# Optimization experiments

Hardware: AMD Instinct MI355X
Metric: run time of the kernel (lower is better)

Reference implementation:

```python
import jax, jax.numpy as jnp
import numpy as np

N_HEADS = 8
HEAD_SIZE = 64
CONTEXT = 256
D_MODEL = 512
MASK_NEG = 1e9


def setup_inputs() -> dict:
    key = jax.random.key(0)
    k1, k2, k3, k4 = jax.random.split(key, 4)
    B, T, D = 2, 4096, D_MODEL
    # Glorot-uniform-ish scales
    def glorot(k, shape):
        fan_in, fan_out = shape[-2], shape[-1]
        lim = jnp.sqrt(6.0 / (fan_in + fan_out))
        return jax.random.uniform(k, shape, jnp.float32, -lim, lim)
    inputs = jax.random.normal(k1, (B, T, D), dtype=jnp.float32)
    WQ = glorot(k2, (N_HEADS, D, HEAD_SIZE))
    WV = glorot(k3, (N_HEADS, D, HEAD_SIZE))
    WU = glorot(k4, (N_HEADS * HEAD_SIZE, D))
    return {"inputs": inputs, "WQ": WQ, "WV": WV, "WU": WU}


def reference(inputs, WQ, WV, WU):
    B, T, D = inputs.shape
    H, _, S = WQ.shape
    # Q, V: [B, H, T, hs]
    Q = jnp.einsum('btd,hds->bhts', inputs, WQ)
    V = jnp.einsum('btd,hds->bhts', inputs, WV)
    # Scores use Q @ V^T (no separate K in this module): [B, H, T, T]
    scores = jnp.einsum('bhts,bhus->bhtu', Q, V) / jnp.sqrt(jnp.float32(S))
    idx = jnp.arange(T)
    band = jnp.abs(idx[:, None] - idx[None, :]) <= CONTEXT  # [T, T] bool
    scores = scores - MASK_NEG * (~band).astype(scores.dtype)
    W = jax.nn.softmax(scores, axis=-1)
    C = jnp.einsum('bhtu,bhus->bhts', W, V)  # [B, H, T, hs]
    # concat heads along feature dim: [B, T, H*hs]
    C = C.transpose(0, 2, 1, 3).reshape(B, T, H * S)
    return C @ WU  # [B, T, D]
```

## Files before the change

### kernel.cpp

```cpp
#include <hip/hip_runtime.h>

#define TSEQ 4096
#define DM 512
#define NH 8
#define HS 64
#define CTX 256

typedef __attribute__((ext_vector_type(8))) short bf16x8;
typedef __attribute__((ext_vector_type(4))) float f32x4;
typedef unsigned short u16;
typedef unsigned long long ull;

__device__ __forceinline__ u16 f2bf(float x) {
    unsigned u = __float_as_uint(x);
    unsigned r = (u + 0x7fffu + ((u >> 16) & 1u)) >> 16;
    return (u16)r;
}
__device__ __forceinline__ float bf2f(u16 b) {
    return __uint_as_float(((unsigned)b) << 16);
}
__device__ __forceinline__ unsigned bf16dup(float p) {
    unsigned w;
    asm("v_cvt_pk_bf16_f32 %0, %1, %1" : "=v"(w) : "v"(p));
    return w;
}
template<int CTRL>
__device__ __forceinline__ float dpp_ror(float x) {
    int xi = __float_as_int(x);
    return __int_as_float(__builtin_amdgcn_update_dpp(xi, xi, CTRL, 0xf, 0xf, false));
}
__device__ __forceinline__ float row16_max(float v) {
    v = fmaxf(v, dpp_ror<0x121>(v));
    v = fmaxf(v, dpp_ror<0x122>(v));
    v = fmaxf(v, dpp_ror<0x124>(v));
    v = fmaxf(v, dpp_ror<0x128>(v));
    return v;
}

#define MFMA(a, b, c) __builtin_amdgcn_mfma_f32_16x16x32_bf16((a), (b), (c), 0, 0, 0)

__global__ __launch_bounds__(256) void presplit_xw(
    const float* __restrict__ X,
    const float* __restrict__ WQ, const float* __restrict__ WV,
    const float* __restrict__ WU,
    u16* __restrict__ Xh,
    u16* __restrict__ WQt_h, u16* __restrict__ WVt_h, u16* __restrict__ WUt_h)
{
    int b = blockIdx.x;
    if (b < 2048) {
        size_t idx = ((size_t)b * 256 + threadIdx.x) * 8;
        float4 p0 = *(const float4*)(X + idx);
        float4 p1 = *(const float4*)(X + idx + 4);
        float v[8] = {p0.x, p0.y, p0.z, p0.w, p1.x, p1.y, p1.z, p1.w};
        bf16x8 h;
        #pragma unroll
        for (int i = 0; i < 8; ++i) h[i] = (short)f2bf(v[i]);
        *(bf16x8*)(Xh + idx) = h;
    } else {
        int gidx = (b - 2048) * 256 + threadIdx.x;
        int a = gidx >> 18;
        int r = gidx & 262143;
        float val;
        u16* dh;
        int dst;
        if (a < 2) {
            int h = r >> 15, s = (r >> 9) & 63, d = r & 511;
            const float* W = (a == 0) ? WQ : WV;
            val = W[h * 32768 + d * 64 + s];
            dst = h * 32768 + s * 512 + d;
            dh = (a == 0) ? WQt_h : WVt_h;
        } else {
            int n = r >> 9, k = r & 511;
            val = WU[k * 512 + n];
            dst = n * 512 + k;
            dh = WUt_h;
        }
        dh[dst] = f2bf(val);
    }
}

__global__ __launch_bounds__(256) void gemm_qv(
    const u16* __restrict__ Ah_g,
    const u16* __restrict__ B0h, const u16* __restrict__ B1h,
    u16* __restrict__ O0h,
    u16* __restrict__ O1h,
    u16* __restrict__ O1t)
{
    __shared__ u16 Ah[128][64];
    __shared__ u16 Bh[64][64];

    const int tid = threadIdx.x;
    const int w = tid >> 6, lane = tid & 63;
    const int lg = lane >> 4, ln = lane & 15;
    const int r0 = blockIdx.x * 128;
    const int y = blockIdx.y;

    const u16* Bsh = (y < 8) ? B0h + (size_t)y * 32768
                             : B1h + (size_t)(y - 8) * 32768;

    const int r_a = tid >> 3;
    const int kc  = tid & 7;
    const int wcol = (kc * 8) ^ ((r_a & 7) << 3);
    const size_t gA = (size_t)(r0 + r_a) * DM + kc * 8;
    const size_t gB = (size_t)r_a * 512 + kc * 8;

    bf16x8 a0h, a1h, a2h, a3h, b0h, b1h;

    #define GLOAD(k0)                                                   \
        a0h = *(const bf16x8*)(Ah_g + gA + (k0));                       \
        a1h = *(const bf16x8*)(Ah_g + gA + 32 * DM + (k0));             \
        a2h = *(const bf16x8*)(Ah_g + gA + 64 * DM + (k0));             \
        a3h = *(const bf16x8*)(Ah_g + gA + 96 * DM + (k0));             \
        b0h = *(const bf16x8*)(Bsh + gB + (k0));                        \
        b1h = *(const bf16x8*)(Bsh + gB + 32 * 512 + (k0));

    f32x4 acc[2][4];
    #pragma unroll
    for (int i = 0; i < 2; ++i)
        #pragma unroll
        for (int j = 0; j < 4; ++j)
            acc[i][j] = (f32x4){0.f, 0.f, 0.f, 0.f};

    GLOAD(0);

    for (int kt = 0; kt < 8; ++kt) {
        __syncthreads();
        *(bf16x8*)&Ah[r_a][wcol]      = a0h;
        *(bf16x8*)&Ah[r_a + 32][wcol] = a1h;
        *(bf16x8*)&Ah[r_a + 64][wcol] = a2h;
        *(bf16x8*)&Ah[r_a + 96][wcol] = a3h;
        *(bf16x8*)&Bh[r_a][wcol]      = b0h;
        *(bf16x8*)&Bh[r_a + 32][wcol] = b1h;
        __syncthreads();
        if (kt < 7) { GLOAD((kt + 1) * 64); }

        #pragma unroll
        for (int kk = 0; kk < 2; ++kk) {
            const int fc = (kk * 32 + lg * 8) ^ ((ln & 7) << 3);
            bf16x8 ah[2], bh2[4];
            #pragma unroll
            for (int ti = 0; ti < 2; ++ti)
                ah[ti] = *(const bf16x8*)&Ah[w * 32 + ti * 16 + ln][fc];
            #pragma unroll
            for (int nj = 0; nj < 4; ++nj)
                bh2[nj] = *(const bf16x8*)&Bh[nj * 16 + ln][fc];
            #pragma unroll
            for (int ti = 0; ti < 2; ++ti)
                #pragma unroll
                for (int nj = 0; nj < 4; ++nj)
                    acc[ti][nj] = MFMA(ah[ti], bh2[nj], acc[ti][nj]);
        }
    }
    #undef GLOAD

    const float qscale = (y < 8) ? 0.18033688f : 1.0f;
    #pragma unroll
    for (int ti = 0; ti < 2; ++ti)
        #pragma unroll
        for (int nj = 0; nj < 4; ++nj) {
            u16 hb[4];
            #pragma unroll
            for (int r = 0; r < 4; ++r) {
                float val = acc[ti][nj][r] * qscale;
                hb[r] = f2bf(val);
                int t = r0 + w * 32 + ti * 16 + lg * 4 + r;
                int n = nj * 16 + ln;
                int bh = (t >> 12) * NH + (y & 7);
                size_t off = ((size_t)bh * TSEQ + (t & (TSEQ - 1))) * HS + n;
                if (y < 8) O0h[off] = hb[r];
                else       O1h[off] = hb[r];
            }
            if (y >= 8) {
                int t = r0 + w * 32 + ti * 16 + lg * 4;
                int n = nj * 16 + ln;
                int bh = (t >> 12) * NH + (y & 7);
                size_t off = (size_t)bh * TSEQ * HS + (size_t)n * TSEQ + (t & (TSEQ - 1));
                ull pk = (ull)hb[0] | ((ull)hb[1] << 16)
                       | ((ull)hb[2] << 32) | ((ull)hb[3] << 48);
                *(ull*)(O1t + off) = pk;
            }
        }
}

__global__ __launch_bounds__(256) void gemm_out(
    const u16* __restrict__ Ah_g, const u16* __restrict__ Bt_h,
    float* __restrict__ Of)
{
    __shared__ u16 Ah[64][64];
    __shared__ u16 Bh[64][64];

    const int tid = threadIdx.x;
    const int w = tid >> 6, lane = tid & 63;
    const int lg = lane >> 4, ln = lane & 15;
    const int r0 = blockIdx.x * 64;
    const int y = blockIdx.y;

    const u16* Bsh = Bt_h + (size_t)y * 64 * 512;

    const int r_a = tid >> 3;
    const int kc  = tid & 7;
    const int wcol = (kc * 8) ^ ((r_a & 7) << 3);
    const size_t gA = (size_t)(r0 + r_a) * DM + kc * 8;
    const size_t gB = (size_t)r_a * 512 + kc * 8;

    bf16x8 a0h, a1h, b0h, b1h;

    #define GLOAD(k0)                                                   \
        a0h = *(const bf16x8*)(Ah_g + gA + (k0));                       \
        a1h = *(const bf16x8*)(Ah_g + gA + 32 * DM + (k0));             \
        b0h = *(const bf16x8*)(Bsh + gB + (k0));                        \
        b1h = *(const bf16x8*)(Bsh + gB + 32 * 512 + (k0));

    f32x4 acc[4];
    #pragma unroll
    for (int j = 0; j < 4; ++j)
        acc[j] = (f32x4){0.f, 0.f, 0.f, 0.f};

    GLOAD(0);

    for (int kt = 0; kt < 8; ++kt) {
        __syncthreads();
        *(bf16x8*)&Ah[r_a][wcol]      = a0h;
        *(bf16x8*)&Ah[r_a + 32][wcol] = a1h;
        *(bf16x8*)&Bh[r_a][wcol]      = b0h;
        *(bf16x8*)&Bh[r_a + 32][wcol] = b1h;
        __syncthreads();
        if (kt < 7) { GLOAD((kt + 1) * 64); }

        #pragma unroll
        for (int kk = 0; kk < 2; ++kk) {
            const int fc = (kk * 32 + lg * 8) ^ ((ln & 7) << 3);
            bf16x8 ah = *(const bf16x8*)&Ah[w * 16 + ln][fc];
            bf16x8 bh2[4];
            #pragma unroll
            for (int nj = 0; nj < 4; ++nj)
                bh2[nj] = *(const bf16x8*)&Bh[nj * 16 + ln][fc];
            #pragma unroll
            for (int nj = 0; nj < 4; ++nj)
                acc[nj] = MFMA(ah, bh2[nj], acc[nj]);
        }
    }
    #undef GLOAD

    #pragma unroll
    for (int nj = 0; nj < 4; ++nj)
        #pragma unroll
        for (int r = 0; r < 4; ++r) {
            int t = r0 + w * 16 + lg * 4 + r;
            Of[(size_t)t * DM + y * 64 + nj * 16 + ln] = acc[nj][r];
        }
}

__global__ __launch_bounds__(256) void attn_v11(
    const u16* __restrict__ Qh_g,
    const u16* __restrict__ Vnh_g, const u16* __restrict__ Vth_g,
    u16* __restrict__ Ch)
{
    __shared__ u16 Vn_h[2][64][64];
    __shared__ u16 Vt_h[2][64][64];
    __shared__ unsigned Ps[4][16][32];

    const int tid = threadIdx.x;
    const int w = tid >> 6, lane = tid & 63;
    const int lg = lane >> 4, ln = lane & 15;
    const int raw = blockIdx.x;
    const int swz = (raw & 7) * 128 + (raw >> 3);
    const int ttile = swz & 63;
    const int bh = swz >> 6;
    const int t0 = ttile * 64;
    const size_t base = (size_t)bh * TSEQ * HS;
    const u16* Qph = Qh_g + base;
    const u16* Vph = Vnh_g + base;
    const u16* Vth = Vth_g + base;

    bf16x8 qh[2];
    #pragma unroll
    for (int kk = 0; kk < 2; ++kk) {
        size_t off = (size_t)(t0 + w * 16 + ln) * HS + kk * 32 + lg * 8;
        qh[kk] = *(const bf16x8*)(Qph + off);
    }

    bf16x8 ones_frag;
    #pragma unroll
    for (int e = 0; e < 8; ++e)
        ones_frag[e] = (ln == 0) ? (short)0x3F80 : (short)0;

    f32x4 o[4], o4;
    float m[4];
    #pragma unroll
    for (int j = 0; j < 4; ++j) {
        o[j] = (f32x4){0.f, 0.f, 0.f, 0.f};
        m[j] = -1e30f;
    }
    o4 = (f32x4){0.f, 0.f, 0.f, 0.f};

    int u_lo = t0 - CTX; if (u_lo < 0) u_lo = 0;
    int u_hi = t0 + 64 + CTX; if (u_hi > TSEQ) u_hi = TSEQ;

    const int sr = tid >> 3;
    const int c8 = (tid & 7) * 8;
    const int wcA = c8 ^ ((sr & 7) << 3);

    bf16x8 vn0h, vn1h, vt0h, vt1h;
    #define VL(u0v)                                                             \
        vn0h = *(const bf16x8*)(Vph + (size_t)((u0v) + sr) * HS + c8);          \
        vn1h = *(const bf16x8*)(Vph + (size_t)((u0v) + sr + 32) * HS + c8);     \
        vt0h = *(const bf16x8*)(Vth + (size_t)sr * TSEQ + (u0v) + c8);          \
        vt1h = *(const bf16x8*)(Vth + (size_t)(sr + 32) * TSEQ + (u0v) + c8);
    #define VSTORE(bufi)                                                        \
        *(bf16x8*)&Vn_h[bufi][sr][wcA]      = vn0h;                             \
        *(bf16x8*)&Vn_h[bufi][sr + 32][wcA] = vn1h;                             \
        *(bf16x8*)&Vt_h[bufi][sr][wcA]      = vt0h;                             \
        *(bf16x8*)&Vt_h[bufi][sr + 32][wcA] = vt1h;

    VL(u_lo);
    VSTORE(0);
    __syncthreads();

    int cur = 0;
    for (int u0 = u_lo; u0 < u_hi; u0 += 64) {
        const bool more = (u0 + 64 < u_hi);
        if (more) { VL(u0 + 64); }

        f32x4 s[4];
        #pragma unroll
        for (int j = 0; j < 4; ++j) s[j] = (f32x4){0.f, 0.f, 0.f, 0.f};

        #pragma unroll
        for (int kk = 0; kk < 2; ++kk) {
            const int fc = (kk * 32 + lg * 8) ^ ((ln & 7) << 3);
            bf16x8 vh[4];
            #pragma unroll
            for (int uj = 0; uj < 4; ++uj)
                vh[uj] = *(const bf16x8*)&Vn_h[cur][uj * 16 + ln][fc];
            #pragma unroll
            for (int uj = 0; uj < 4; ++uj)
                s[uj] = MFMA(qh[kk], vh[uj], s[uj]);
        }

        bool needmask = ((t0 + 63 - u0) > CTX) || ((u0 + 63 - t0) > CTX);
        if (needmask) {
            #pragma unroll
            for (int uj = 0; uj < 4; ++uj)
                #pragma unroll
                for (int r = 0; r < 4; ++r) {
                    int t = t0 + w * 16 + lg * 4 + r;
                    int u = u0 + uj * 16 + ln;
                    int d = t - u; if (d < 0) d = -d;
                    if (d > CTX) s[uj][r] = -1e30f;
                }
        }

        float rm[4];
        bool need = false;
        #pragma unroll
        for (int r = 0; r < 4; ++r) {
            float v = fmaxf(fmaxf(s[0][r], s[1][r]), fmaxf(s[2][r], s[3][r]));
            rm[r] = row16_max(v);
            need |= (rm[r] > m[r] + 8.f);
        }
        if (__any(need)) {
            #pragma unroll
            for (int r = 0; r < 4; ++r) {
                float mn = fmaxf(m[r], rm[r]);
                float sc2 = exp2f(m[r] - mn);
                m[r] = mn;
                o4[r] *= sc2;
                #pragma unroll
                for (int sj = 0; sj < 4; ++sj)
                    o[sj][r] *= sc2;
            }
        }
        #pragma unroll
        for (int r = 0; r < 4; ++r)
            #pragma unroll
            for (int uj = 0; uj < 4; ++uj)
                s[uj][r] = exp2f(s[uj][r] - m[r]);

        #pragma unroll
        for (int kk = 0; kk < 2; ++kk) {
            #pragma unroll
            for (int u2 = 0; u2 < 2; ++u2) {
                int uj = kk * 2 + u2;
                #pragma unroll
                for (int r = 0; r < 4; ++r) {
                    int trow = lg * 4 + r;
                    int ucol = (u2 * 16 + ln) ^ ((trow & 7) << 2);
                    Ps[w][trow][ucol] = bf16dup(s[uj][r]);
                }
            }

            bf16x8 ph, vth4[4];
            {
                int sw = (ln & 7) << 2;
                uint4 q0 = *(const uint4*)&Ps[w][ln][(lg * 8) ^ sw];
                uint4 q1 = *(const uint4*)&Ps[w][ln][(lg * 8 + 4) ^ sw];
                union { unsigned u[4]; bf16x8 v; } H;
                H.u[0] = __builtin_amdgcn_perm(q0.y, q0.x, 0x05040100u);
                H.u[1] = __builtin_amdgcn_perm(q0.w, q0.z, 0x05040100u);
                H.u[2] = __builtin_amdgcn_perm(q1.y, q1.x, 0x05040100u);
                H.u[3] = __builtin_amdgcn_perm(q1.w, q1.z, 0x05040100u);
                ph = H.v;
            }
            const int fct = (kk * 32 + lg * 8) ^ ((ln & 7) << 3);
            #pragma unroll
            for (int sj = 0; sj < 4; ++sj)
                vth4[sj] = *(const bf16x8*)&Vt_h[cur][sj * 16 + ln][fct];
            #pragma unroll
            for (int sj = 0; sj < 4; ++sj)
                o[sj] = MFMA(ph, vth4[sj], o[sj]);
            o4 = MFMA(ph, ones_frag, o4);
        }

        if (more) { VSTORE(cur ^ 1); }
        __syncthreads();
        cur ^= 1;
    }
    #undef VL
    #undef VSTORE

    const int b = bh >> 3, h = bh & 7;
    #pragma unroll
    for (int r = 0; r < 4; ++r) {
        float ls = __shfl(o4[r], (lane >> 4) << 4);
        float inv = 1.f / ls;
        int t = t0 + w * 16 + lg * 4 + r;
        #pragma unroll
        for (int sj = 0; sj < 4; ++sj) {
            int ss = sj * 16 + ln;
            float val = o[sj][r] * inv;
            size_t off = ((size_t)(b * TSEQ + t)) * DM + h * HS + ss;
            Ch[off] = f2bf(val);
        }
    }
}

extern "C" void kernel_launch(void* const* d_in, const int* in_sizes, int n_in,
                              void* d_out, int out_size, void* d_ws, size_t ws_size,
                              hipStream_t stream) {
    const float* X  = (const float*)d_in[0];
    const float* WQ = (const float*)d_in[1];
    const float* WV = (const float*)d_in[2];
    const float* WU = (const float*)d_in[3];
    float* out = (float*)d_out;

    const size_t SZ = 8388608;
    char* ws = (char*)d_ws;

    u16* Xh = (u16*)(ws);
    u16* Qh = (u16*)(ws + 2 * SZ);
    u16* Vh = (u16*)(ws + 4 * SZ);
    u16* Vth = (u16*)(ws + 6 * SZ);
    char* wsw = ws + 8 * SZ;
    u16* WQt_h = (u16*)(wsw);
    u16* WVt_h = (u16*)(wsw + 524288);
    u16* WUt_h = (u16*)(wsw + 2 * 524288);

    presplit_xw<<<5120, 256, 0, stream>>>(X, WQ, WV, WU, Xh, WQt_h, WVt_h, WUt_h);
    gemm_qv<<<dim3(64, 16), 256, 0, stream>>>(Xh, WQt_h, WVt_h, Qh, Vh, Vth);
    attn_v11<<<1024, 256, 0, stream>>>(Qh, Vh, Vth, Xh);
    gemm_out<<<dim3(128, 8), 256, 0, stream>>>(Xh, WUt_h, out);
}
```

Baseline: 72.17 us.

## Compute Q and V projections in one block sharing the X tile

The Q/V projection GEMM is reorganized so each block loads a 64-row X tile once and multiplies it against both the WQ and WV head slices, instead of launching separate blocks for Q and V that each reload 128 X rows. The grid becomes 128x8 with smaller row tiles, and each wave computes 16 rows times 64 columns for both Q and V. This is meant to halve X tile traffic and remove the divergent branches in the epilogue. The cost is less A-fragment reuse per wave across row tiles and more LDS traffic for B fragments.

```diff
diff --git a/kernel.cpp b/kernel.cpp
--- a/kernel.cpp
+++ b/kernel.cpp
@@ -79,24 +79,25 @@
     }
 }
 
-__global__ __launch_bounds__(256) void gemm_qv(
+__global__ __launch_bounds__(256) void gemm_qv2(
     const u16* __restrict__ Ah_g,
-    const u16* __restrict__ B0h, const u16* __restrict__ B1h,
-    u16* __restrict__ O0h,
-    u16* __restrict__ O1h,
-    u16* __restrict__ O1t)
+    const u16* __restrict__ BQ, const u16* __restrict__ BV,
+    u16* __restrict__ Qh,
+    u16* __restrict__ Vh,
+    u16* __restrict__ Vt)
 {
-    __shared__ u16 Ah[128][64];
-    __shared__ u16 Bh[64][64];
+    __shared__ u16 Ah[64][64];
+    __shared__ u16 Bq[64][64];
+    __shared__ u16 Bv[64][64];
 
     const int tid = threadIdx.x;
     const int w = tid >> 6, lane = tid & 63;
     const int lg = lane >> 4, ln = lane & 15;
-    const int r0 = blockIdx.x * 128;
+    const int r0 = blockIdx.x * 64;
     const int y = blockIdx.y;
 
-    const u16* Bsh = (y < 8) ? B0h + (size_t)y * 32768
-                             : B1h + (size_t)(y - 8) * 32768;
+    const u16* Bq_g = BQ + (size_t)y * 32768;
+    const u16* Bv_g = BV + (size_t)y * 32768;
 
     const int r_a = tid >> 3;
     const int kc  = tid & 7;
@@ -104,22 +105,22 @@
     const size_t gA = (size_t)(r0 + r_a) * DM + kc * 8;
     const size_t gB = (size_t)r_a * 512 + kc * 8;
 
-    bf16x8 a0h, a1h, a2h, a3h, b0h, b1h;
+    bf16x8 a0h, a1h, q0h, q1h, v0h, v1h;
 
     #define GLOAD(k0)                                                   \
         a0h = *(const bf16x8*)(Ah_g + gA + (k0));                       \
         a1h = *(const bf16x8*)(Ah_g + gA + 32 * DM + (k0));             \
-        a2h = *(const bf16x8*)(Ah_g + gA + 64 * DM + (k0));             \
-        a3h = *(const bf16x8*)(Ah_g + gA + 96 * DM + (k0));             \
-        b0h = *(const bf16x8*)(Bsh + gB + (k0));                        \
-        b1h = *(const bf16x8*)(Bsh + gB + 32 * 512 + (k0));
-
-    f32x4 acc[2][4];
-    #pragma unroll
-    for (int i = 0; i < 2; ++i)
-        #pragma unroll
-        for (int j = 0; j < 4; ++j)
-            acc[i][j] = (f32x4){0.f, 0.f, 0.f, 0.f};
+        q0h = *(const bf16x8*)(Bq_g + gB + (k0));                       \
+        q1h = *(const bf16x8*)(Bq_g + gB + 32 * 512 + (k0));            \
+        v0h = *(const bf16x8*)(Bv_g + gB + (k0));                       \
+        v1h = *(const bf16x8*)(Bv_g + gB + 32 * 512 + (k0));
+
+    f32x4 accq[4], accv[4];
+    #pragma unroll
+    for (int j = 0; j < 4; ++j) {
+        accq[j] = (f32x4){0.f, 0.f, 0.f, 0.f};
+        accv[j] = (f32x4){0.f, 0.f, 0.f, 0.f};
+    }
 
     GLOAD(0);
 
@@ -127,59 +128,57 @@
         __syncthreads();
         *(bf16x8*)&Ah[r_a][wcol]      = a0h;
         *(bf16x8*)&Ah[r_a + 32][wcol] = a1h;
-        *(bf16x8*)&Ah[r_a + 64][wcol] = a2h;
-        *(bf16x8*)&Ah[r_a + 96][wcol] = a3h;
-        *(bf16x8*)&Bh[r_a][wcol]      = b0h;
-        *(bf16x8*)&Bh[r_a + 32][wcol] = b1h;
+        *(bf16x8*)&Bq[r_a][wcol]      = q0h;
+        *(bf16x8*)&Bq[r_a + 32][wcol] = q1h;
+        *(bf16x8*)&Bv[r_a][wcol]      = v0h;
+        *(bf16x8*)&Bv[r_a + 32][wcol] = v1h;
         __syncthreads();
         if (kt < 7) { GLOAD((kt + 1) * 64); }
 
         #pragma unroll
         for (int kk = 0; kk < 2; ++kk) {
             const int fc = (kk * 32 + lg * 8) ^ ((ln & 7) << 3);
-            bf16x8 ah[2], bh2[4];
-            #pragma unroll
-            for (int ti = 0; ti < 2; ++ti)
-                ah[ti] = *(const bf16x8*)&Ah[w * 32 + ti * 16 + ln][fc];
-            #pragma unroll
-            for (int nj = 0; nj < 4; ++nj)
-                bh2[nj] = *(const bf16x8*)&Bh[nj * 16 + ln][fc];
-            #pragma unroll
-            for (int ti = 0; ti < 2; ++ti)
-                #pragma unroll
-                for (int nj = 0; nj < 4; ++nj)
-                    acc[ti][nj] = MFMA(ah[ti], bh2[nj], acc[ti][nj]);
+            bf16x8 ah = *(const bf16x8*)&Ah[w * 16 + ln][fc];
+            bf16x8 bq2[4], bv2[4];
+            #pragma unroll
+            for (int nj = 0; nj < 4; ++nj) {
+                bq2[nj] = *(const bf16x8*)&Bq[nj * 16 + ln][fc];
+                bv2[nj] = *(const bf16x8*)&Bv[nj * 16 + ln][fc];
+            }
+            #pragma unroll
+            for (int nj = 0; nj < 4; ++nj) {
+                accq[nj] = MFMA(ah, bq2[nj], accq[nj]);
+                accv[nj] = MFMA(ah, bv2[nj], accv[nj]);
+            }
         }
     }
     #undef GLOAD
 
-    const float qscale = (y < 8) ? 0.18033688f : 1.0f;
-    #pragma unroll
-    for (int ti = 0; ti < 2; ++ti)
-        #pragma unroll
-        for (int nj = 0; nj < 4; ++nj) {
-            u16 hb[4];
-            #pragma unroll
-            for (int r = 0; r < 4; ++r) {
-                float val = acc[ti][nj][r] * qscale;
-                hb[r] = f2bf(val);
-                int t = r0 + w * 32 + ti * 16 + lg * 4 + r;
-                int n = nj * 16 + ln;
-                int bh = (t >> 12) * NH + (y & 7);
-                size_t off = ((size_t)bh * TSEQ + (t & (TSEQ - 1))) * HS + n;
-                if (y < 8) O0h[off] = hb[r];
-                else       O1h[off] = hb[r];
-            }
-            if (y >= 8) {
-                int t = r0 + w * 32 + ti * 16 + lg * 4;
-                int n = nj * 16 + ln;
-                int bh = (t >> 12) * NH + (y & 7);
-                size_t off = (size_t)bh * TSEQ * HS + (size_t)n * TSEQ + (t & (TSEQ - 1));
-                ull pk = (ull)hb[0] | ((ull)hb[1] << 16)
-                       | ((ull)hb[2] << 32) | ((ull)hb[3] << 48);
-                *(ull*)(O1t + off) = pk;
-            }
-        }
+    const float qscale = 0.18033688f;
+    const int tb = r0 + w * 16 + lg * 4;
+    const int bh = (tb >> 12) * NH + y;
+    const size_t obase = (size_t)bh * TSEQ * HS;
+    #pragma unroll
+    for (int nj = 0; nj < 4; ++nj) {
+        int n = nj * 16 + ln;
+        u16 hb[4];
+        #pragma unroll
+        for (int r = 0; r < 4; ++r) {
+            int t = tb + r;
+            Qh[obase + (size_t)(t & (TSEQ - 1)) * HS + n] =
+                f2bf(accq[nj][r] * qscale);
+        }
+        #pragma unroll
+        for (int r = 0; r < 4; ++r) {
+            hb[r] = f2bf(accv[nj][r]);
+            int t = tb + r;
+            Vh[obase + (size_t)(t & (TSEQ - 1)) * HS + n] = hb[r];
+        }
+        size_t toff = obase + (size_t)n * TSEQ + (tb & (TSEQ - 1));
+        ull pk = (ull)hb[0] | ((ull)hb[1] << 16)
+               | ((ull)hb[2] << 32) | ((ull)hb[3] << 48);
+        *(ull*)(Vt + toff) = pk;
+    }
 }
 
 __global__ __launch_bounds__(256) void gemm_out(
@@ -457,7 +456,7 @@
     u16* WUt_h = (u16*)(wsw + 2 * 524288);
 
     presplit_xw<<<5120, 256, 0, stream>>>(X, WQ, WV, WU, Xh, WQt_h, WVt_h, WUt_h);
-    gemm_qv<<<dim3(64, 16), 256, 0, stream>>>(Xh, WQt_h, WVt_h, Qh, Vh, Vth);
+    gemm_qv2<<<dim3(128, 8), 256, 0, stream>>>(Xh, WQt_h, WVt_h, Qh, Vh, Vth);
     attn_v11<<<1024, 256, 0, stream>>>(Qh, Vh, Vth, Xh);
     gemm_out<<<dim3(128, 8), 256, 0, stream>>>(Xh, WUt_h, out);
 }
```

Measured after the change: 72.97 us. About the same (+1.1%).
